# Optimization experiments

Measured on AMD Instinct MI355X. Metric: run time of the kernel, lower is better.

Reference implementation:

```python
import jax, jax.numpy as jnp
import numpy as np

EMBED_DIM = 64
B, H, S, D = 2, 16, 2048, EMBED_DIM


def setup_inputs() -> dict:
    key = jax.random.key(0)
    ks = jax.random.split(key, 5)
    shp = (B, H, S, D)
    return {
        "Q": jax.random.normal(ks[0], shp, dtype=jnp.float32),
        "K": jax.random.normal(ks[1], shp, dtype=jnp.float32),
        "V": jax.random.normal(ks[2], shp, dtype=jnp.float32),
        "Q_position": jax.random.normal(ks[3], shp, dtype=jnp.float32),
        "K_position": jax.random.normal(ks[4], shp, dtype=jnp.float32),
    }


def reference(Q, K, V, Q_position, K_position):
    scale = 1.0 / np.sqrt(EMBED_DIM).astype(np.float32)
    # content scores + positional similarity, both scaled by 1/sqrt(d)
    scores = jnp.einsum("bhqd,bhkd->bhqk", Q, K) * scale
    scores = scores + jnp.einsum("bhqd,bhkd->bhqk", Q_position, K_position) * scale
    attn = jax.nn.softmax(scores, axis=-1)
    context = jnp.einsum("bhqk,bhkd->bhqd", attn, V)
    return context
```

## Files before the change

kernel.cpp:

```cpp
#include <hip/hip_runtime.h>

#define BH_ 32
#define S_ 2048
#define D_ 64
#define DQK 128
#define BQ 256

typedef unsigned short u16;
typedef unsigned int u32;
typedef u16 u16x8 __attribute__((ext_vector_type(8)));
typedef u32 u32x4 __attribute__((ext_vector_type(4)));
typedef __bf16 bf16x8 __attribute__((ext_vector_type(8)));
typedef float f32x16 __attribute__((ext_vector_type(16)));

__device__ __forceinline__ u16 f2bf_rne(float f) {
  unsigned u = __builtin_bit_cast(unsigned, f);
  u += 0x7fffu + ((u >> 16) & 1u);
  return (u16)(u >> 16);
}
__device__ __forceinline__ bf16x8 ld8(const u16* p) {
  return __builtin_bit_cast(bf16x8, *(const u16x8*)p);
}
__device__ __forceinline__ void g2l16(const u16* g, u16* l) {
  __builtin_amdgcn_global_load_lds(
      (const __attribute__((address_space(1))) unsigned int*)g,
      (__attribute__((address_space(3))) unsigned int*)l, 16, 0, 0);
}
__device__ __forceinline__ u32 cvtpk(float lo, float hi) {
  u32 r;
  asm("v_cvt_pk_bf16_f32 %0, %1, %2" : "=v"(r) : "v"(lo), "v"(hi));
  return r;
}
__device__ __forceinline__ void swap32(u32& a, u32& b) {
  asm("v_permlane32_swap_b32 %0, %1" : "+v"(a), "+v"(b));
}
__device__ __forceinline__ f32x16 zero16() {
  f32x16 z;
  #pragma unroll
  for (int i = 0; i < 16; ++i) z[i] = 0.f;
  return z;
}

#define COEF 0.1803368801111204f

__global__ __launch_bounds__(256)
void prep_kernel(const float* __restrict__ K, const float* __restrict__ V,
                 const float* __restrict__ Kp,
                 u16* __restrict__ Kc, u16* __restrict__ Vt) {
  __shared__ float Ls[64][65];
  int b = blockIdx.x;
  if (b < 4096) {
    int t = b * 256 + threadIdx.x;
    int kv    = t & 63;
    int chunk = (t >> 6) & 15;
    int kt    = (t >> 10) & 31;
    int bh    = t >> 15;
    int s     = kt * 64 + kv;
    int col8  = chunk * 8;
    const float* src = (col8 < 64) ? (K  + ((size_t)bh * S_ + s) * D_ + col8)
                                   : (Kp + ((size_t)bh * S_ + s) * D_ + (col8 - 64));
    float4 v0 = *(const float4*)src;
    float4 v1 = *(const float4*)(src + 4);
    u16x8 w;
    w[0] = f2bf_rne(v0.x); w[1] = f2bf_rne(v0.y); w[2] = f2bf_rne(v0.z); w[3] = f2bf_rne(v0.w);
    w[4] = f2bf_rne(v1.x); w[5] = f2bf_rne(v1.y); w[6] = f2bf_rne(v1.z); w[7] = f2bf_rne(v1.w);
    *(u16x8*)(Kc + ((((size_t)bh * 32 + kt) * 16 + chunk) * 64 + kv) * 8) = w;
  } else {
    int id = b - 4096;
    int bh = id >> 5, kt = id & 31;
    int tid = threadIdx.x;
    #pragma unroll
    for (int it = 0; it < 4; ++it) {
      int i = it * 256 + tid;
      int kv = i >> 4, dg = (i & 15) * 4;
      float4 v = *(const float4*)(V + ((size_t)bh * S_ + kt * 64 + kv) * D_ + dg);
      Ls[kv][dg + 0] = v.x; Ls[kv][dg + 1] = v.y;
      Ls[kv][dg + 2] = v.z; Ls[kv][dg + 3] = v.w;
    }
    __syncthreads();
    int d = tid >> 2, kvg = (tid & 3) * 16;
    u16x8 w0, w1;
    #pragma unroll
    for (int j = 0; j < 8; ++j) w0[j] = f2bf_rne(Ls[kvg + j][d]);
    #pragma unroll
    for (int j = 0; j < 8; ++j) w1[j] = f2bf_rne(Ls[kvg + 8 + j][d]);
    u16* base = Vt + ((size_t)bh * 32 + kt) * 4096;
    int c = (tid & 3) * 2;
    *(u16x8*)(base + ((size_t)(c * 64 + d)) * 8)       = w0;
    *(u16x8*)(base + ((size_t)((c + 1) * 64 + d)) * 8) = w1;
  }
}

template <int SPLIT>
__global__ __launch_bounds__(512, 4)
void fa3_kernel(const float* __restrict__ Q, const float* __restrict__ Qp,
                const u16* __restrict__ Kc, const u16* __restrict__ Vtg,
                float* __restrict__ out, float* __restrict__ Opart,
                float* __restrict__ lpart) {
  __shared__ alignas(16) u16 Ks[3][8192];
  __shared__ alignas(16) u16 Vs[3][4096];

  const int tid  = threadIdx.x;
  const int wave = tid >> 6;
  const int lane = tid & 63;
  const int l32  = lane & 31;
  const int hi   = lane >> 5;

  const int id   = blockIdx.x;
  const int p    = SPLIT ? (id & 63) : (id & 31);
  const int qblk = SPLIT ? (id >> 6) : (id >> 5);
  const int bh   = p & 31;
  const int kz   = SPLIT ? (p >> 5) : 0;

  const int qw = qblk * BQ + wave * 32;
  const int kt0 = kz * 16;
  const int NKT = SPLIT ? 16 : 32;

  bf16x8 bq[8];
  #pragma unroll
  for (int kstep = 0; kstep < 8; ++kstep) {
    int k0 = kstep * 16 + hi * 8;
    const float* src = (k0 < 64)
        ? (Q  + ((size_t)bh * S_ + qw + l32) * D_ + k0)
        : (Qp + ((size_t)bh * S_ + qw + l32) * D_ + (k0 - 64));
    float4 v0 = *(const float4*)src;
    float4 v1 = *(const float4*)(src + 4);
    u16x8 w;
    w[0] = f2bf_rne(v0.x * COEF); w[1] = f2bf_rne(v0.y * COEF);
    w[2] = f2bf_rne(v0.z * COEF); w[3] = f2bf_rne(v0.w * COEF);
    w[4] = f2bf_rne(v1.x * COEF); w[5] = f2bf_rne(v1.y * COEF);
    w[6] = f2bf_rne(v1.z * COEF); w[7] = f2bf_rne(v1.w * COEF);
    bq[kstep] = __builtin_bit_cast(bf16x8, w);
  }

  const u16* kcp = Kc  + ((size_t)bh * 32 + kt0) * 8192 + tid * 8;
  const u16* vtp = Vtg + ((size_t)bh * 32 + kt0) * 4096 + tid * 8;

  #pragma unroll
  for (int j = 0; j < 2; ++j) g2l16(kcp + j * 4096, &Ks[0][0] + tid * 8 + j * 4096);
  g2l16(vtp, &Vs[0][0] + tid * 8);
  #pragma unroll
  for (int j = 0; j < 2; ++j) g2l16(kcp + 8192 + j * 4096, &Ks[1][0] + tid * 8 + j * 4096);
  g2l16(vtp + 4096, &Vs[1][0] + tid * 8);

  f32x16 accd[2];
  accd[0] = zero16(); accd[1] = zero16();
  float l_part = 0.f;

  int cur = 0;
  for (int kt = 0; kt < NKT; ++kt) {
    if (kt == NKT - 1) asm volatile("s_waitcnt vmcnt(0)" ::: "memory");
    else               asm volatile("s_waitcnt vmcnt(3)" ::: "memory");
    __builtin_amdgcn_s_barrier();
    if (kt + 2 < NKT) {
      int nx = cur + 2; if (nx >= 3) nx -= 3;
      const u16* kg = kcp + (size_t)(kt + 2) * 8192;
      u16* kl = &Ks[nx][0] + tid * 8;
      #pragma unroll
      for (int j = 0; j < 2; ++j) g2l16(kg + j * 4096, kl + j * 4096);
      g2l16(vtp + (size_t)(kt + 2) * 4096, &Vs[nx][0] + tid * 8);
    }
    __builtin_amdgcn_sched_barrier(0);

    const u16* ksb = &Ks[cur][0];
    const u16* vsb = &Vs[cur][0];

    f32x16 s[2];
    s[0] = zero16(); s[1] = zero16();
    #pragma unroll
    for (int kstep = 0; kstep < 8; ++kstep) {
      bf16x8 akA = ld8(ksb + (((kstep * 2 + hi) * 64) + l32) * 8);
      bf16x8 akB = ld8(ksb + (((kstep * 2 + hi) * 64) + 32 + l32) * 8);
      s[0] = __builtin_amdgcn_mfma_f32_32x32x16_bf16(akA, bq[kstep], s[0], 0, 0, 0);
      s[1] = __builtin_amdgcn_mfma_f32_32x32x16_bf16(akB, bq[kstep], s[1], 0, 0, 0);
    }

    #pragma unroll
    for (int h = 0; h < 2; ++h) {
      float rs0 = 0.f, rs1 = 0.f;
      #pragma unroll
      for (int r = 0; r < 8; ++r) {
        float e0 = __builtin_amdgcn_exp2f(s[h][r]);
        float e1 = __builtin_amdgcn_exp2f(s[h][8 + r]);
        s[h][r] = e0; s[h][8 + r] = e1;
        rs0 += e0; rs1 += e1;
      }
      l_part += rs0 + rs1;
      #pragma unroll
      for (int k2 = 0; k2 < 2; ++k2) {
        u32 a0 = cvtpk(s[h][8 * k2 + 0], s[h][8 * k2 + 1]);
        u32 b0 = cvtpk(s[h][8 * k2 + 4], s[h][8 * k2 + 5]);
        swap32(a0, b0);
        u32 a1 = cvtpk(s[h][8 * k2 + 2], s[h][8 * k2 + 3]);
        u32 b1 = cvtpk(s[h][8 * k2 + 6], s[h][8 * k2 + 7]);
        swap32(a1, b1);
        u32x4 pw; pw[0] = a0; pw[1] = a1; pw[2] = b0; pw[3] = b1;
        bf16x8 pa = __builtin_bit_cast(bf16x8, pw);
        int ksl = 2 * h + k2;
        #pragma unroll
        for (int dt = 0; dt < 2; ++dt) {
          bf16x8 bv = ld8(vsb + (((ksl * 2 + hi) * 64) + dt * 32 + l32) * 8);
          accd[dt] = __builtin_amdgcn_mfma_f32_32x32x16_bf16(pa, bv, accd[dt], 0, 0, 0);
        }
      }
    }
    cur = (cur == 2) ? 0 : cur + 1;
  }

  float lsum = l_part + __shfl_xor(l_part, 32);

  if (SPLIT) {
    #pragma unroll
    for (int r = 0; r < 16; ++r) {
      int qrow = (r & 3) + 8 * (r >> 2) + 4 * hi;
      size_t rowb = ((size_t)kz * 65536 + (size_t)bh * S_ + qw + qrow) * D_;
      Opart[rowb + l32]      = accd[0][r];
      Opart[rowb + 32 + l32] = accd[1][r];
    }
    if (hi == 0)
      lpart[(size_t)kz * 65536 + (size_t)bh * S_ + qw + l32] = lsum;
  } else {
    #pragma unroll
    for (int r = 0; r < 16; ++r) {
      int qrow = (r & 3) + 8 * (r >> 2) + 4 * hi;
      float inv = 1.0f / __shfl(lsum, qrow);
      size_t rowb = ((size_t)bh * S_ + qw + qrow) * D_;
      out[rowb + l32]      = accd[0][r] * inv;
      out[rowb + 32 + l32] = accd[1][r] * inv;
    }
  }
}

__global__ __launch_bounds__(256)
void combine_kernel(const float* __restrict__ Opart, const float* __restrict__ lpart,
                    float* __restrict__ out) {
  int t = blockIdx.x * 256 + threadIdx.x;
  int row = t >> 4;
  int d4  = (t & 15) * 4;
  float4 o0 = *(const float4*)(Opart + (size_t)row * D_ + d4);
  float4 o1 = *(const float4*)(Opart + (size_t)65536 * D_ + (size_t)row * D_ + d4);
  float inv = 1.0f / (lpart[row] + lpart[65536 + row]);
  float4 o;
  o.x = (o0.x + o1.x) * inv; o.y = (o0.y + o1.y) * inv;
  o.z = (o0.z + o1.z) * inv; o.w = (o0.w + o1.w) * inv;
  *(float4*)(out + (size_t)row * D_ + d4) = o;
}

extern "C" void kernel_launch(void* const* d_in, const int* in_sizes, int n_in,
                              void* d_out, int out_size, void* d_ws, size_t ws_size,
                              hipStream_t stream) {
  const float* Q  = (const float*)d_in[0];
  const float* K  = (const float*)d_in[1];
  const float* V  = (const float*)d_in[2];
  const float* Qp = (const float*)d_in[3];
  const float* Kp = (const float*)d_in[4];
  float* out = (float*)d_out;

  const size_t nKc = (size_t)BH_ * S_ * DQK;
  const size_t nVt = (size_t)BH_ * S_ * D_;
  const size_t nO  = (size_t)2 * 65536 * D_;
  const size_t nL  = (size_t)2 * 65536;
  const size_t needSplit = (nO + nL) * 4 + (nKc + nVt) * 2;

  if (ws_size >= needSplit) {
    float* Opart = (float*)d_ws;
    float* lpart = Opart + nO;
    u16* Kc = (u16*)(lpart + nL);
    u16* Vt = Kc + nKc;
    prep_kernel<<<dim3(4096 + 1024), dim3(256), 0, stream>>>(K, V, Kp, Kc, Vt);
    fa3_kernel<1><<<dim3((S_ / BQ) * BH_ * 2), dim3(512), 0, stream>>>(Q, Qp, Kc, Vt, nullptr, Opart, lpart);
    combine_kernel<<<dim3(4096), dim3(256), 0, stream>>>(Opart, lpart, out);
  } else {
    u16* Kc = (u16*)d_ws;
    u16* Vt = Kc + nKc;
    prep_kernel<<<dim3(4096 + 1024), dim3(256), 0, stream>>>(K, V, Kp, Kc, Vt);
    fa3_kernel<0><<<dim3((S_ / BQ) * BH_), dim3(512), 0, stream>>>(Q, Qp, Kc, Vt, out, nullptr, nullptr);
  }
}
```

Measured before the change: 181.9 us.

## Process two 32-row query groups per wave with 256-thread blocks

Each wave now handles 64 query rows (two 32-row groups) instead of 32, and blocks shrink from 512 to 256 threads while keeping the same 256-row query block. Each K/V fragment read from LDS is reused for two MFMAs, which halves LDS reads per MFMA and gives more independent MFMA chains per wave. The cost is roughly double the register use for accumulators, scores and Q fragments, and fewer waves per CU to hide latency. Global-to-LDS loads are split into more issues per thread, with the wait count adjusted to match.

After: 176.6 us. 1.03x faster.

```diff
diff --git a/kernel.cpp b/kernel.cpp
--- a/kernel.cpp
+++ b/kernel.cpp
@@ -92,7 +92,7 @@
 }
 
 template <int SPLIT>
-__global__ __launch_bounds__(512, 4)
+__global__ __launch_bounds__(256, 2)
 void fa3_kernel(const float* __restrict__ Q, const float* __restrict__ Qp,
                 const u16* __restrict__ Kc, const u16* __restrict__ Vtg,
                 float* __restrict__ out, float* __restrict__ Opart,
@@ -112,121 +112,144 @@
   const int bh   = p & 31;
   const int kz   = SPLIT ? (p >> 5) : 0;
 
-  const int qw = qblk * BQ + wave * 32;
+  const int qw = qblk * BQ + wave * 64;
   const int kt0 = kz * 16;
   const int NKT = SPLIT ? 16 : 32;
 
-  bf16x8 bq[8];
-  #pragma unroll
-  for (int kstep = 0; kstep < 8; ++kstep) {
-    int k0 = kstep * 16 + hi * 8;
-    const float* src = (k0 < 64)
-        ? (Q  + ((size_t)bh * S_ + qw + l32) * D_ + k0)
-        : (Qp + ((size_t)bh * S_ + qw + l32) * D_ + (k0 - 64));
-    float4 v0 = *(const float4*)src;
-    float4 v1 = *(const float4*)(src + 4);
-    u16x8 w;
-    w[0] = f2bf_rne(v0.x * COEF); w[1] = f2bf_rne(v0.y * COEF);
-    w[2] = f2bf_rne(v0.z * COEF); w[3] = f2bf_rne(v0.w * COEF);
-    w[4] = f2bf_rne(v1.x * COEF); w[5] = f2bf_rne(v1.y * COEF);
-    w[6] = f2bf_rne(v1.z * COEF); w[7] = f2bf_rne(v1.w * COEF);
-    bq[kstep] = __builtin_bit_cast(bf16x8, w);
-  }
+  bf16x8 bq[2][8];
+  #pragma unroll
+  for (int g = 0; g < 2; ++g)
+    #pragma unroll
+    for (int kstep = 0; kstep < 8; ++kstep) {
+      int k0 = kstep * 16 + hi * 8;
+      const float* src = (k0 < 64)
+          ? (Q  + ((size_t)bh * S_ + qw + g * 32 + l32) * D_ + k0)
+          : (Qp + ((size_t)bh * S_ + qw + g * 32 + l32) * D_ + (k0 - 64));
+      float4 v0 = *(const float4*)src;
+      float4 v1 = *(const float4*)(src + 4);
+      u16x8 w;
+      w[0] = f2bf_rne(v0.x * COEF); w[1] = f2bf_rne(v0.y * COEF);
+      w[2] = f2bf_rne(v0.z * COEF); w[3] = f2bf_rne(v0.w * COEF);
+      w[4] = f2bf_rne(v1.x * COEF); w[5] = f2bf_rne(v1.y * COEF);
+      w[6] = f2bf_rne(v1.z * COEF); w[7] = f2bf_rne(v1.w * COEF);
+      bq[g][kstep] = __builtin_bit_cast(bf16x8, w);
+    }
 
   const u16* kcp = Kc  + ((size_t)bh * 32 + kt0) * 8192 + tid * 8;
   const u16* vtp = Vtg + ((size_t)bh * 32 + kt0) * 4096 + tid * 8;
 
   #pragma unroll
-  for (int j = 0; j < 2; ++j) g2l16(kcp + j * 4096, &Ks[0][0] + tid * 8 + j * 4096);
-  g2l16(vtp, &Vs[0][0] + tid * 8);
-  #pragma unroll
-  for (int j = 0; j < 2; ++j) g2l16(kcp + 8192 + j * 4096, &Ks[1][0] + tid * 8 + j * 4096);
-  g2l16(vtp + 4096, &Vs[1][0] + tid * 8);
-
-  f32x16 accd[2];
-  accd[0] = zero16(); accd[1] = zero16();
-  float l_part = 0.f;
+  for (int j = 0; j < 4; ++j) g2l16(kcp + j * 2048, &Ks[0][0] + tid * 8 + j * 2048);
+  #pragma unroll
+  for (int j = 0; j < 2; ++j) g2l16(vtp + j * 2048, &Vs[0][0] + tid * 8 + j * 2048);
+  #pragma unroll
+  for (int j = 0; j < 4; ++j) g2l16(kcp + 8192 + j * 2048, &Ks[1][0] + tid * 8 + j * 2048);
+  #pragma unroll
+  for (int j = 0; j < 2; ++j) g2l16(vtp + 4096 + j * 2048, &Vs[1][0] + tid * 8 + j * 2048);
+
+  f32x16 accd[2][2];
+  #pragma unroll
+  for (int g = 0; g < 2; ++g) { accd[g][0] = zero16(); accd[g][1] = zero16(); }
+  float l_part[2] = {0.f, 0.f};
 
   int cur = 0;
   for (int kt = 0; kt < NKT; ++kt) {
     if (kt == NKT - 1) asm volatile("s_waitcnt vmcnt(0)" ::: "memory");
-    else               asm volatile("s_waitcnt vmcnt(3)" ::: "memory");
+    else               asm volatile("s_waitcnt vmcnt(6)" ::: "memory");
     __builtin_amdgcn_s_barrier();
     if (kt + 2 < NKT) {
       int nx = cur + 2; if (nx >= 3) nx -= 3;
       const u16* kg = kcp + (size_t)(kt + 2) * 8192;
       u16* kl = &Ks[nx][0] + tid * 8;
       #pragma unroll
-      for (int j = 0; j < 2; ++j) g2l16(kg + j * 4096, kl + j * 4096);
-      g2l16(vtp + (size_t)(kt + 2) * 4096, &Vs[nx][0] + tid * 8);
+      for (int j = 0; j < 4; ++j) g2l16(kg + j * 2048, kl + j * 2048);
+      const u16* vg = vtp + (size_t)(kt + 2) * 4096;
+      u16* vl = &Vs[nx][0] + tid * 8;
+      #pragma unroll
+      for (int j = 0; j < 2; ++j) g2l16(vg + j * 2048, vl + j * 2048);
     }
     __builtin_amdgcn_sched_barrier(0);
 
     const u16* ksb = &Ks[cur][0];
     const u16* vsb = &Vs[cur][0];
 
-    f32x16 s[2];
-    s[0] = zero16(); s[1] = zero16();
+    f32x16 s[2][2];
+    #pragma unroll
+    for (int g = 0; g < 2; ++g) { s[g][0] = zero16(); s[g][1] = zero16(); }
     #pragma unroll
     for (int kstep = 0; kstep < 8; ++kstep) {
       bf16x8 akA = ld8(ksb + (((kstep * 2 + hi) * 64) + l32) * 8);
       bf16x8 akB = ld8(ksb + (((kstep * 2 + hi) * 64) + 32 + l32) * 8);
-      s[0] = __builtin_amdgcn_mfma_f32_32x32x16_bf16(akA, bq[kstep], s[0], 0, 0, 0);
-      s[1] = __builtin_amdgcn_mfma_f32_32x32x16_bf16(akB, bq[kstep], s[1], 0, 0, 0);
+      #pragma unroll
+      for (int g = 0; g < 2; ++g) {
+        s[g][0] = __builtin_amdgcn_mfma_f32_32x32x16_bf16(akA, bq[g][kstep], s[g][0], 0, 0, 0);
+        s[g][1] = __builtin_amdgcn_mfma_f32_32x32x16_bf16(akB, bq[g][kstep], s[g][1], 0, 0, 0);
+      }
     }
 
     #pragma unroll
     for (int h = 0; h < 2; ++h) {
-      float rs0 = 0.f, rs1 = 0.f;
-      #pragma unroll
-      for (int r = 0; r < 8; ++r) {
-        float e0 = __builtin_amdgcn_exp2f(s[h][r]);
-        float e1 = __builtin_amdgcn_exp2f(s[h][8 + r]);
-        s[h][r] = e0; s[h][8 + r] = e1;
-        rs0 += e0; rs1 += e1;
-      }
-      l_part += rs0 + rs1;
+      #pragma unroll
+      for (int g = 0; g < 2; ++g) {
+        float rs0 = 0.f, rs1 = 0.f;
+        #pragma unroll
+        for (int r = 0; r < 8; ++r) {
+          float e0 = __builtin_amdgcn_exp2f(s[g][h][r]);
+          float e1 = __builtin_amdgcn_exp2f(s[g][h][8 + r]);
+          s[g][h][r] = e0; s[g][h][8 + r] = e1;
+          rs0 += e0; rs1 += e1;
+        }
+        l_part[g] += rs0 + rs1;
+      }
       #pragma unroll
       for (int k2 = 0; k2 < 2; ++k2) {
-        u32 a0 = cvtpk(s[h][8 * k2 + 0], s[h][8 * k2 + 1]);
-        u32 b0 = cvtpk(s[h][8 * k2 + 4], s[h][8 * k2 + 5]);
-        swap32(a0, b0);
-        u32 a1 = cvtpk(s[h][8 * k2 + 2], s[h][8 * k2 + 3]);
-        u32 b1 = cvtpk(s[h][8 * k2 + 6], s[h][8 * k2 + 7]);
-        swap32(a1, b1);
-        u32x4 pw; pw[0] = a0; pw[1] = a1; pw[2] = b0; pw[3] = b1;
-        bf16x8 pa = __builtin_bit_cast(bf16x8, pw);
+        bf16x8 pa[2];
+        #pragma unroll
+        for (int g = 0; g < 2; ++g) {
+          u32 a0 = cvtpk(s[g][h][8 * k2 + 0], s[g][h][8 * k2 + 1]);
+          u32 b0 = cvtpk(s[g][h][8 * k2 + 4], s[g][h][8 * k2 + 5]);
+          swap32(a0, b0);
+          u32 a1 = cvtpk(s[g][h][8 * k2 + 2], s[g][h][8 * k2 + 3]);
+          u32 b1 = cvtpk(s[g][h][8 * k2 + 6], s[g][h][8 * k2 + 7]);
+          swap32(a1, b1);
+          u32x4 pw; pw[0] = a0; pw[1] = a1; pw[2] = b0; pw[3] = b1;
+          pa[g] = __builtin_bit_cast(bf16x8, pw);
+        }
         int ksl = 2 * h + k2;
         #pragma unroll
         for (int dt = 0; dt < 2; ++dt) {
           bf16x8 bv = ld8(vsb + (((ksl * 2 + hi) * 64) + dt * 32 + l32) * 8);
-          accd[dt] = __builtin_amdgcn_mfma_f32_32x32x16_bf16(pa, bv, accd[dt], 0, 0, 0);
+          #pragma unroll
+          for (int g = 0; g < 2; ++g)
+            accd[g][dt] = __builtin_amdgcn_mfma_f32_32x32x16_bf16(pa[g], bv, accd[g][dt], 0, 0, 0);
         }
       }
     }
     cur = (cur == 2) ? 0 : cur + 1;
   }
 
-  float lsum = l_part + __shfl_xor(l_part, 32);
-
-  if (SPLIT) {
-    #pragma unroll
-    for (int r = 0; r < 16; ++r) {
-      int qrow = (r & 3) + 8 * (r >> 2) + 4 * hi;
-      size_t rowb = ((size_t)kz * 65536 + (size_t)bh * S_ + qw + qrow) * D_;
-      Opart[rowb + l32]      = accd[0][r];
-      Opart[rowb + 32 + l32] = accd[1][r];
-    }
-    if (hi == 0)
-      lpart[(size_t)kz * 65536 + (size_t)bh * S_ + qw + l32] = lsum;
-  } else {
-    #pragma unroll
-    for (int r = 0; r < 16; ++r) {
-      int qrow = (r & 3) + 8 * (r >> 2) + 4 * hi;
-      float inv = 1.0f / __shfl(lsum, qrow);
-      size_t rowb = ((size_t)bh * S_ + qw + qrow) * D_;
-      out[rowb + l32]      = accd[0][r] * inv;
-      out[rowb + 32 + l32] = accd[1][r] * inv;
+  #pragma unroll
+  for (int g = 0; g < 2; ++g) {
+    float lsum = l_part[g] + __shfl_xor(l_part[g], 32);
+    if (SPLIT) {
+      #pragma unroll
+      for (int r = 0; r < 16; ++r) {
+        int qrow = (r & 3) + 8 * (r >> 2) + 4 * hi;
+        size_t rowb = ((size_t)kz * 65536 + (size_t)bh * S_ + qw + g * 32 + qrow) * D_;
+        Opart[rowb + l32]      = accd[g][0][r];
+        Opart[rowb + 32 + l32] = accd[g][1][r];
+      }
+      if (hi == 0)
+        lpart[(size_t)kz * 65536 + (size_t)bh * S_ + qw + g * 32 + l32] = lsum;
+    } else {
+      #pragma unroll
+      for (int r = 0; r < 16; ++r) {
+        int qrow = (r & 3) + 8 * (r >> 2) + 4 * hi;
+        float inv = 1.0f / __shfl(lsum, qrow);
+        size_t rowb = ((size_t)bh * S_ + qw + g * 32 + qrow) * D_;
+        out[rowb + l32]      = accd[g][0][r] * inv;
+        out[rowb + 32 + l32] = accd[g][1][r] * inv;
+      }
     }
   }
 }
@@ -268,12 +291,12 @@
     u16* Kc = (u16*)(lpart + nL);
     u16* Vt = Kc + nKc;
     prep_kernel<<<dim3(4096 + 1024), dim3(256), 0, stream>>>(K, V, Kp, Kc, Vt);
-    fa3_kernel<1><<<dim3((S_ / BQ) * BH_ * 2), dim3(512), 0, stream>>>(Q, Qp, Kc, Vt, nullptr, Opart, lpart);
+    fa3_kernel<1><<<dim3((S_ / BQ) * BH_ * 2), dim3(256), 0, stream>>>(Q, Qp, Kc, Vt, nullptr, Opart, lpart);
     combine_kernel<<<dim3(4096), dim3(256), 0, stream>>>(Opart, lpart, out);
   } else {
     u16* Kc = (u16*)d_ws;
     u16* Vt = Kc + nKc;
     prep_kernel<<<dim3(4096 + 1024), dim3(256), 0, stream>>>(K, V, Kp, Kc, Vt);
-    fa3_kernel<0><<<dim3((S_ / BQ) * BH_), dim3(512), 0, stream>>>(Q, Qp, Kc, Vt, out, nullptr, nullptr);
+    fa3_kernel<0><<<dim3((S_ / BQ) * BH_), dim3(256), 0, stream>>>(Q, Qp, Kc, Vt, out, nullptr, nullptr);
   }
 }
```
